# Performance work log

Measured on AMD Instinct MI355X. Metric: run time of the kernel, lower is better.

The kernel has to match this reference:

```python
import jax, jax.numpy as jnp
import numpy as np

B = 4          # clouds per batch
N_PER = 8192   # points per cloud
RATIO = 0.5
M = int(N_PER * RATIO)   # sampled centroids per cloud
R = 0.2        # radius
K = 64         # max_num_neighbors
C_IN = 64


def setup_inputs() -> dict:
    key = jax.random.key(0)
    k1, k2, k3, k4 = jax.random.split(key, 4)
    N = B * N_PER
    x = jax.random.normal(k1, (N, C_IN), dtype=jnp.float32)
    pos = jax.random.uniform(k2, (N, 3), dtype=jnp.float32)  # unit cube
    batch = jnp.repeat(jnp.arange(B, dtype=jnp.int32), N_PER)
    W1 = jax.random.normal(k3, (C_IN + 3, 64), dtype=jnp.float32) * (1.0 / np.sqrt(C_IN + 3))
    b1 = jnp.zeros((64,), dtype=jnp.float32)
    W2 = jax.random.normal(k4, (64, 128), dtype=jnp.float32) * (1.0 / np.sqrt(64))
    b2 = jnp.zeros((128,), dtype=jnp.float32)
    return {"x": x, "pos": pos, "batch": batch, "W1": W1, "b1": b1, "W2": W2, "b2": b2}


def _fps(posb):
    """Farthest point sampling, vectorized over clouds. posb: [B, n, 3] -> idx [B, M]."""
    d0 = jnp.sum((posb - posb[:, :1]) ** 2, axis=-1)  # dist^2 to seed point 0: [B, n]

    def step(dists, _):
        far = jnp.argmax(dists, axis=1)                              # [B]
        newp = jnp.take_along_axis(posb, far[:, None, None], axis=1)  # [B, 1, 3]
        d = jnp.sum((posb - newp) ** 2, axis=-1)                      # [B, n]
        return jnp.minimum(dists, d), far.astype(jnp.int32)

    _, rest = jax.lax.scan(step, d0, None, length=M - 1)  # rest: [M-1, B]
    return jnp.concatenate([jnp.zeros((B, 1), jnp.int32), rest.T], axis=1)  # [B, M]


def reference(x, pos, batch, W1, b1, W2, b2):
    posb = pos.reshape(B, N_PER, 3)
    xb = x.reshape(B, N_PER, C_IN)

    # --- fps ---
    idx = _fps(posb)                                         # [B, M]
    q = jnp.take_along_axis(posb, idx[:, :, None], axis=1)   # sampled centroids [B, M, 3]

    # --- radius query: K nearest neighbors within radius R (same cloud) ---
    d2 = jnp.sum((q[:, :, None, :] - posb[:, None, :, :]) ** 2, axis=-1)  # [B, M, n]
    neg = jnp.where(d2 <= R * R, -d2, -jnp.inf)
    vals, nbr = jax.lax.top_k(neg, K)                        # [B, M, K]
    valid = vals > -jnp.inf                                  # neighbor mask

    # --- PointNetConv: gather -> MLP -> masked max aggregation ---
    bidx = jnp.arange(B)[:, None, None]
    xj = xb[bidx, nbr]                                       # [B, M, K, C_IN]
    rel = posb[bidx, nbr] - q[:, :, None, :]                 # [B, M, K, 3]
    feat = jnp.concatenate([xj, rel], axis=-1)               # [B, M, K, C_IN+3]
    h = jax.nn.relu(feat @ W1 + b1)                          # [B, M, K, 64]
    h = jax.nn.relu(h @ W2 + b2)                             # [B, M, K, 128]
    h = jnp.where(valid[..., None], h, -jnp.inf)
    out = jnp.max(h, axis=2)                                 # [B, M, 128]; self-edge guarantees >=1 valid

    x_out = out.reshape(B * M, 128)
    pos_out = q.reshape(B * M, 3)
    batch_out = jnp.repeat(jnp.arange(B, dtype=batch.dtype), M)
    return x_out, pos_out, batch_out
```

## Files before the change

kernel.cpp:

```cpp
#include <hip/hip_runtime.h>
#include <stdint.h>

#define NPER 8192
#define NB 4
#define MPER 4096
#define MTOT (NB*MPER)
#define KNB 64
#define CIN 64
#define R2C 0.04f

#define POSOUT_OFF (MTOT*128)
#define BATCH_OFF  (MTOT*128 + MTOT*3)

#define PRE_OFF 2162688ull
#define PRE_BYTES 8388608ull

#define SSTR 34816
#define PERM_F 29200

typedef float v2f __attribute__((ext_vector_type(2)));

#define FPS_T 1024
#define PTS 8
#define NCELL 512

#define OFF_XS 0
#define OFF_YS (OFF_XS + NPER*4)
#define OFF_ZS (OFF_YS + NPER*4)
#define OFF_OS (OFF_ZS + NPER*4)
#define OFF_WIN (OFF_OS + NPER*2)
#define OFF_HIST (OFF_WIN + MPER*2)
#define OFF_SCAN (OFF_HIST + NCELL*4)
#define OFF_SLOT (OFF_SCAN + NCELL*4)
#define OFF_SID0 (OFF_SLOT + 24)
#define OFF_BSC  (OFF_SID0 + 8)
#define FPS_LDS  (OFF_BSC + NCELL*4)

template<int CTRL>
__device__ __forceinline__ unsigned dppmax(unsigned v) {
  unsigned t = (unsigned)__builtin_amdgcn_update_dpp(
      0, (int)v, CTRL, 0xf, 0xf, true);
  return v > t ? v : t;
}
__device__ __forceinline__ unsigned wave_max_u32(unsigned v) {
  v = dppmax<0x111>(v);
  v = dppmax<0x112>(v);
  v = dppmax<0x114>(v);
  v = dppmax<0x118>(v);
  v = dppmax<0x142>(v);
  v = dppmax<0x143>(v);
  return (unsigned)__builtin_amdgcn_readlane((int)v, 63);
}

__device__ __forceinline__ unsigned brick_key(unsigned c) {
  unsigned ix = c >> 6, iy = (c >> 3) & 7, iz = c & 7;
  unsigned bid = ((ix >> 2) << 3) | ((iy >> 2) << 2) | (iz >> 1);
  unsigned lid = ((ix & 3) << 3) | ((iy & 3) << 1) | (iz & 1);
  return (bid << 5) | lid;
}

__global__ __launch_bounds__(1024) void k_fps(const float* __restrict__ pos,
                                              float* __restrict__ dout)
{
#pragma clang fp contract(off)
  extern __shared__ char smem[];
  float* Xs = (float*)(smem + OFF_XS);
  float* Ys = (float*)(smem + OFF_YS);
  float* Zs = (float*)(smem + OFF_ZS);
  unsigned short* Os = (unsigned short*)(smem + OFF_OS);
  unsigned short* winb = (unsigned short*)(smem + OFF_WIN);
  unsigned* hist = (unsigned*)(smem + OFF_HIST);
  unsigned* scanb = (unsigned*)(smem + OFF_SCAN);
  unsigned long long* slot3 = (unsigned long long*)(smem + OFF_SLOT);
  unsigned* sid0p = (unsigned*)(smem + OFF_SID0);
  unsigned* bsc = (unsigned*)(smem + OFF_BSC);

  const int b = blockIdx.x;
  const int tid = threadIdx.x;
  const float* pb = pos + (size_t)b * NPER * 3;
  float* qo = dout + POSOUT_OFF + (size_t)b * MPER * 3;
  float* scrb = dout + (size_t)b * SSTR;
  float* gSX = scrb; float* gSY = scrb + 8192; float* gSZ = scrb + 16384;
  unsigned* gSO = (unsigned*)(scrb + 24576);
  unsigned* gCS = (unsigned*)(scrb + 28672);
  unsigned short* gPM = (unsigned short*)(scrb + PERM_F);

  if (tid < NCELL) hist[tid] = 0u;
  if (tid == 0) { slot3[0] = 0ull; slot3[1] = 0ull; slot3[2] = 0ull; }
  __syncthreads();

  float sxv[PTS], syv[PTS], szv[PTS];
  unsigned cellv[PTS];
#pragma unroll
  for (int k = 0; k < PTS; ++k) {
    int i = k * FPS_T + tid;
    sxv[k] = pb[i*3+0]; syv[k] = pb[i*3+1]; szv[k] = pb[i*3+2];
    unsigned ix = min(7u, (unsigned)(int)(sxv[k] * 8.0f));
    unsigned iy = min(7u, (unsigned)(int)(syv[k] * 8.0f));
    unsigned iz = min(7u, (unsigned)(int)(szv[k] * 8.0f));
    cellv[k] = (ix << 6) | (iy << 3) | iz;
    atomicAdd(&hist[cellv[k]], 1u);
  }
  __syncthreads();
  if (tid < NCELL) scanb[tid] = hist[tid];
  __syncthreads();
  for (int s = 1; s < NCELL; s <<= 1) {
    unsigned v = 0u;
    if (tid >= s && tid < NCELL) v = scanb[tid - s];
    __syncthreads();
    if (tid >= s && tid < NCELL) scanb[tid] += v;
    __syncthreads();
  }
  if (tid < NCELL) {
    hist[tid] = scanb[tid] - hist[tid];
    gCS[tid+1] = scanb[tid];
  }
  if (tid == 0) gCS[0] = 0u;
  __syncthreads();
  if (tid < NCELL) {
    unsigned c = (unsigned)tid;
    unsigned cntc = scanb[c] - hist[c];
    bsc[brick_key(c)] = cntc;
  }
  __syncthreads();
  for (int s = 1; s < NCELL; s <<= 1) {
    unsigned v = 0u;
    if (tid >= s && tid < NCELL) v = bsc[tid - s];
    __syncthreads();
    if (tid >= s && tid < NCELL) bsc[tid] += v;
    __syncthreads();
  }
  {
    unsigned bst = 0u;
    if (tid < NCELL) {
      unsigned c = (unsigned)tid;
      unsigned cntc = scanb[c] - hist[c];
      bst = bsc[brick_key(c)] - cntc;
    }
    __syncthreads();
    if (tid < NCELL) bsc[tid] = bst;
  }
  __syncthreads();
#pragma unroll
  for (int k = 0; k < PTS; ++k) {
    unsigned dst = atomicAdd(&hist[cellv[k]], 1u);
    unsigned p   = atomicAdd(&bsc[cellv[k]], 1u);
    int orig = k * FPS_T + tid;
    Xs[dst] = sxv[k]; Ys[dst] = syv[k]; Zs[dst] = szv[k];
    Os[dst] = (unsigned short)orig;
    gPM[p] = (unsigned short)dst;
    if (orig == 0) *sid0p = dst;
  }
  __syncthreads();
  for (int e = tid; e < NPER; e += FPS_T) {
    gSX[e] = Xs[e]; gSY[e] = Ys[e]; gSZ[e] = Zs[e];
  }
  for (int e = tid; e < NPER/2; e += FPS_T)
    gSO[e] = ((const unsigned*)Os)[e];
  v2f Xp[4], Yp[4], Zp[4], Dp[4];
  unsigned RK[PTS];
  float bxlo = 3.402823466e+38f, bylo = bxlo, bzlo = bxlo;
  float bxhi = -bxlo, byhi = bxhi, bzhi = bxhi;
#pragma unroll
  for (int k = 0; k < PTS; ++k) {
    int s = (int)gPM[tid * PTS + k];
    float xx = Xs[s], yy = Ys[s], zz = Zs[s];
    Xp[k>>1][k&1] = xx; Yp[k>>1][k&1] = yy; Zp[k>>1][k&1] = zz;
    Dp[k>>1][k&1] = 3.402823466e+38f;
    unsigned orig = Os[s];
    RK[k] = ((unsigned)(NPER - 1 - orig) << 13) | (unsigned)s;
    bxlo = fminf(bxlo, xx); bxhi = fmaxf(bxhi, xx);
    bylo = fminf(bylo, yy); byhi = fmaxf(byhi, yy);
    bzlo = fminf(bzlo, zz); bzhi = fmaxf(bzhi, zz);
  }

  unsigned long long tkey = 0ull, wkey = 0ull;
  float lmax = 3.402823466e+38f;
  unsigned sidx = *sid0p;
  for (int m = 1; m < MPER; ++m) {
    const float cx = Xs[sidx], cy = Ys[sidx], cz = Zs[sidx];
    if (tid == 0) winb[m-1] = (unsigned short)sidx;
    if (tid == 1) slot3[(m+1) % 3] = 0ull;
    float ax = fmaxf(fmaxf(__fsub_rn(bxlo, cx), __fsub_rn(cx, bxhi)), 0.0f);
    float ay = fmaxf(fmaxf(__fsub_rn(bylo, cy), __fsub_rn(cy, byhi)), 0.0f);
    float az = fmaxf(fmaxf(__fsub_rn(bzlo, cz), __fsub_rn(cz, bzhi)), 0.0f);
    float lb = ax*ax + ay*ay + az*az;
    bool upd = (lb * 0.99988f) < lmax;
    if (__ballot(upd) != 0ull) {
      if (upd) {
        v2f cx2 = {cx, cx}, cy2 = {cy, cy}, cz2 = {cz, cz};
        v2f dnp[4];
        float bd = -1.0f;
#pragma unroll
        for (int p = 0; p < 4; ++p) {
          v2f dx = Xp[p] - cx2;
          v2f dy = Yp[p] - cy2;
          v2f dz = Zp[p] - cz2;
          v2f s = (dx*dx + dy*dy) + dz*dz;
          v2f dn;
          dn.x = fminf(Dp[p].x, s.x);
          dn.y = fminf(Dp[p].y, s.y);
          Dp[p] = dn; dnp[p] = dn;
          bd = fmaxf(bd, fmaxf(dn.x, dn.y));
        }
        unsigned brk = 0u;
#pragma unroll
        for (int p = 0; p < 4; ++p) {
          brk = (dnp[p].x == bd) ? max(brk, RK[2*p])   : brk;
          brk = (dnp[p].y == bd) ? max(brk, RK[2*p+1]) : brk;
        }
        tkey = ((unsigned long long)__float_as_uint(bd) << 26) | brk;
        lmax = bd;
      }
      unsigned hi = (unsigned)(tkey >> 26);
      unsigned M = wave_max_u32(hi);
      unsigned rk = (unsigned)tkey & 0x3FFFFFFu;
      unsigned long long msk = __ballot(hi == M);
      unsigned lo;
      if (__popcll(msk) == 1) {
        int ln = (int)__builtin_ctzll(msk);
        lo = (unsigned)__builtin_amdgcn_readlane((int)rk, ln);
      } else {
        lo = wave_max_u32((hi == M) ? rk : 0u);
      }
      wkey = ((unsigned long long)M << 26) | lo;
    }
    if ((tid & 63) == 0) atomicMax(&slot3[m % 3], wkey);
    __syncthreads();
    sidx = (unsigned)(slot3[m % 3] & 0x1FFFull);
  }
  if (tid == 0) winb[MPER-1] = (unsigned short)sidx;
  __syncthreads();
  for (int e = tid; e < MPER; e += FPS_T) {
    unsigned s = winb[e];
    qo[e*3+0] = Xs[s]; qo[e*3+1] = Ys[s]; qo[e*3+2] = Zs[s];
  }
}

#define SCAP 512
__global__ __launch_bounds__(256) void k_radius(const float* __restrict__ pos,
    float* __restrict__ dout, unsigned short* __restrict__ nbr,
    int* __restrict__ cnt)
{
  __shared__ unsigned candH[4][SCAP];
  __shared__ unsigned candL[4][SCAP];
  const int wid = threadIdx.x >> 6, lane = threadIdx.x & 63;
  const int m = blockIdx.x * 4 + wid;
  const int b = m >> 12;
  const float* scrb = dout + (size_t)b * SSTR;
  const float* SX = scrb;
  const float* SY = scrb + 8192;
  const float* SZ = scrb + 16384;
  const unsigned short* SO = (const unsigned short*)(scrb + 24576);
  const unsigned* CS = (const unsigned*)(scrb + 28672);
  const float* q = dout + POSOUT_OFF + (size_t)m * 3;
  const float qx = q[0], qy = q[1], qz = q[2];
  const int ixc = min(7, (int)(qx * 8.0f));
  const int iyc = min(7, (int)(qy * 8.0f));
  const int izc = min(7, (int)(qz * 8.0f));
  const int izlo = max(izc-2, 0), izhi = min(izc+2, 7);
  unsigned s0v = 0u, s1v = 0u;
  {
    int ix = ixc + lane / 5 - 2;
    int iy = iyc + lane % 5 - 2;
    if (lane < 25 && ix >= 0 && ix < 8 && iy >= 0 && iy < 8) {
      int cb = (ix << 6) | (iy << 3);
      s0v = CS[cb + izlo];
      s1v = CS[cb + izhi + 1];
    }
  }
  unsigned cw = 0;
  for (int seg = 0; seg < 25; ++seg) {
    unsigned s0 = (unsigned)__builtin_amdgcn_readlane((int)s0v, seg);
    unsigned s1 = (unsigned)__builtin_amdgcn_readlane((int)s1v, seg);
    for (unsigned i0 = s0; i0 < s1; i0 += 64) {
      unsigned i = i0 + (unsigned)lane;
      float dx = __fsub_rn(qx, SX[i]);
      float dy = __fsub_rn(qy, SY[i]);
      float dz = __fsub_rn(qz, SZ[i]);
      float d2 = __fadd_rn(__fadd_rn(__fmul_rn(dx,dx), __fmul_rn(dy,dy)),
                           __fmul_rn(dz,dz));
      bool in = (i < s1) && (d2 <= R2C);
      unsigned long long mk = __ballot(in);
      unsigned pre = (unsigned)__popcll(mk & ((1ull << lane) - 1ull));
      if (in) {
        unsigned slot = cw + pre;
        if (slot < SCAP) {
          candH[wid][slot] = __float_as_uint(d2);
          candL[wid][slot] = (unsigned)SO[i];
        }
      }
      cw += (unsigned)__popcll(mk);
    }
  }
  if (cw > SCAP) cw = SCAP;
  for (int s = (int)cw + lane; s < SCAP; s += 64) {
    candH[wid][s] = 0xFFFFFFFFu; candL[wid][s] = 0xFFFFFFFFu;
  }
  __syncthreads();
  for (int k = 2; k <= SCAP; k <<= 1) {
    for (int j = k >> 1; j > 0; j >>= 1) {
#pragma unroll
      for (int s = 0; s < SCAP/128; ++s) {
        int t = lane + (s << 6);
        int e = ((t & ~(j-1)) << 1) | (t & (j-1));
        int p = e | j;
        unsigned aH = candH[wid][e], aL = candL[wid][e];
        unsigned cH = candH[wid][p], cL = candL[wid][p];
        bool agt = (aH > cH) || (aH == cH && aL > cL);
        bool asc = ((e & k) == 0);
        bool sw = asc ? agt : !agt && (aH != cH || aL != cL);
        if (sw) {
          candH[wid][e] = cH; candL[wid][e] = cL;
          candH[wid][p] = aH; candL[wid][p] = aL;
        }
      }
      __syncthreads();
    }
  }
  int kk = (int)cw; if (kk > KNB) kk = KNB;
  nbr[(size_t)m*KNB + lane] =
    (lane < kk) ? (unsigned short)(candL[wid][lane] & 0xFFFFu)
                : (unsigned short)0;
  if (lane == 0) {
    cnt[m] = kk;
    dout[BATCH_OFF + m] = (float)b;
  }
}

__global__ __launch_bounds__(256) void k_pre(const float* __restrict__ x,
    const float* __restrict__ W1, float* __restrict__ hp)
{
  __shared__ float Ws[64*64];
  __shared__ float Xs[64][65];
  const int t = threadIdx.x;
  const int row0 = blockIdx.x * 64;
  for (int e = t; e < 64*64; e += 256) Ws[e] = W1[e];
  for (int e = t; e < 64*64; e += 256) {
    int r = e >> 6, ch = e & 63;
    Xs[r][ch] = x[(size_t)(row0 + r) * 64 + ch];
  }
  __syncthreads();
  const int rg = t >> 4, cg = t & 15;
  const int r0 = rg << 2, c0 = cg << 2;
  float acc[4][4];
#pragma unroll
  for (int r = 0; r < 4; ++r)
#pragma unroll
    for (int c = 0; c < 4; ++c) acc[r][c] = 0.0f;
  for (int k = 0; k < 64; ++k) {
    const float4 w = *(const float4*)&Ws[(k << 6) + c0];
    const float xr[4] = {Xs[r0][k], Xs[r0+1][k], Xs[r0+2][k], Xs[r0+3][k]};
    const float wc[4] = {w.x, w.y, w.z, w.w};
#pragma unroll
    for (int r = 0; r < 4; ++r)
#pragma unroll
      for (int c = 0; c < 4; ++c)
        acc[r][c] = fmaf(xr[r], wc[c], acc[r][c]);
  }
#pragma unroll
  for (int r = 0; r < 4; ++r) {
    float4 o = {acc[r][0], acc[r][1], acc[r][2], acc[r][3]};
    *(float4*)&hp[(size_t)(row0 + r0 + r) * 64 + c0] = o;
  }
}

__global__ __launch_bounds__(128) void k_conv2(
    const float* __restrict__ hp, const float* __restrict__ pos,
    const float* __restrict__ W1, const float* __restrict__ b1,
    const float* __restrict__ W2, const float* __restrict__ b2,
    const unsigned short* __restrict__ nbr, const int* __restrict__ cntp,
    float* __restrict__ dout)
{
  __shared__ __align__(16) float bufA[68*68];
  __shared__ __align__(16) float bufB[16*136];
  __shared__ float w1p[3*64];
  __shared__ unsigned short nbr_s[64];
  __shared__ float qv[3];
  __shared__ int cnt_s;
  const int t = threadIdx.x;
  const int m = blockIdx.x;
  const int b = m >> 12;
  if (t < 64) nbr_s[t] = nbr[(size_t)m*KNB + t];
  else if (t == 64) cnt_s = cntp[m];
  else if (t >= 65 && t < 68) qv[t-65] = dout[POSOUT_OFF + (size_t)m*3 + (t-65)];
  for (int e = t; e < 192; e += 128) w1p[e] = W1[64*64 + e];
  __syncthreads();
  {
    const int h = t & 63, jj = t >> 6;
    const size_t hb = (size_t)b * NPER * 64;
    for (int j0 = 0; j0 < 64; j0 += 2) {
      int j = j0 + jj;
      int r = nbr_s[j];
      bufA[h*68 + j] = hp[hb + (size_t)r*64 + h];
    }
  }
  {
    const size_t pbb = (size_t)b * NPER * 3;
    for (int e = t; e < 192; e += 128) {
      int j = e & 63, d = e >> 6;
      int r = nbr_s[j];
      bufA[(64+d)*68 + j] = pos[pbb + (size_t)r*3 + d] - qv[d];
    }
  }
  __syncthreads();
  for (int e = t; e < 64*64; e += 128) {
    int h = e >> 6, j = e & 63;
    float v = bufA[h*68 + j];
    v = fmaf(bufA[64*68 + j], w1p[h],       v);
    v = fmaf(bufA[65*68 + j], w1p[64 + h],  v);
    v = fmaf(bufA[66*68 + j], w1p[128 + h], v);
    bufA[h*68 + j] = fmaxf(v + b1[h], 0.0f);
  }
  const int jg = t & 7, hg = t >> 3;
  const int j0 = jg << 3;
  const int c0 = hg << 3;
  v2f acc2p[8][4];
#pragma unroll
  for (int c = 0; c < 8; ++c)
#pragma unroll
    for (int jp = 0; jp < 4; ++jp) acc2p[c][jp] = (v2f){0.0f, 0.0f};
  for (int hc = 0; hc < 64; hc += 16) {
    __syncthreads();
    for (int e = t; e < 16*128; e += 128) {
      int hh = e >> 7, c = e & 127;
      bufB[hh*136 + c] = W2[(size_t)(hc+hh)*128 + c];
    }
    __syncthreads();
#pragma unroll
    for (int h = 0; h < 16; ++h) {
      const float4 ja = *(const float4*)&bufA[(hc+h)*68 + j0];
      const float4 jb = *(const float4*)&bufA[(hc+h)*68 + j0 + 4];
      const float4 wa = *(const float4*)&bufB[h*136 + c0];
      const float4 wb = *(const float4*)&bufB[h*136 + c0 + 4];
      const v2f hj[4] = {{ja.x, ja.y}, {ja.z, ja.w}, {jb.x, jb.y}, {jb.z, jb.w}};
      const float wv[8] = {wa.x, wa.y, wa.z, wa.w, wb.x, wb.y, wb.z, wb.w};
#pragma unroll
      for (int c = 0; c < 8; ++c) {
        const v2f w2 = {wv[c], wv[c]};
#pragma unroll
        for (int jp = 0; jp < 4; ++jp)
          acc2p[c][jp] += w2 * hj[jp];
      }
    }
  }
  const int cntv = cnt_s;
  const float4 b2a = *(const float4*)&b2[c0];
  const float4 b2b = *(const float4*)&b2[c0 + 4];
  const float bv2[8] = {b2a.x, b2a.y, b2a.z, b2a.w, b2b.x, b2b.y, b2b.z, b2b.w};
  float best[8];
#pragma unroll
  for (int c = 0; c < 8; ++c) {
    float v = -3.402823466e+38f;
#pragma unroll
    for (int jp = 0; jp < 4; ++jp) {
      float h0v = fmaxf(acc2p[c][jp].x + bv2[c], 0.0f);
      float h1v = fmaxf(acc2p[c][jp].y + bv2[c], 0.0f);
      v = (j0 + 2*jp     < cntv) ? fmaxf(v, h0v) : v;
      v = (j0 + 2*jp + 1 < cntv) ? fmaxf(v, h1v) : v;
    }
    best[c] = v;
  }
#pragma unroll
  for (int off = 1; off < 8; off <<= 1)
#pragma unroll
    for (int c = 0; c < 8; ++c)
      best[c] = fmaxf(best[c], __shfl_xor(best[c], off));
  if (jg == 0) {
    float4 o0 = {best[0], best[1], best[2], best[3]};
    float4 o1 = {best[4], best[5], best[6], best[7]};
    *(float4*)&dout[(size_t)m*128 + c0] = o0;
    *(float4*)&dout[(size_t)m*128 + c0 + 4] = o1;
  }
}

__global__ __launch_bounds__(128) void k_conv(
    const float* __restrict__ x, const float* __restrict__ pos,
    const float* __restrict__ W1, const float* __restrict__ b1,
    const float* __restrict__ W2, const float* __restrict__ b2,
    const unsigned short* __restrict__ nbr, const int* __restrict__ cntp,
    float* __restrict__ dout)
{
  __shared__ __align__(16) float bufA[68*68];
  __shared__ __align__(16) float bufB[68*68];
  __shared__ unsigned short nbr_s[64];
  __shared__ float qv[3];
  __shared__ int cnt_s;
  const int t = threadIdx.x;
  const int m = blockIdx.x;
  const int b = m >> 12;
  if (t < 64) nbr_s[t] = nbr[(size_t)m*KNB + t];
  else if (t == 64) cnt_s = cntp[m];
  else if (t >= 65 && t < 68) qv[t-65] = dout[POSOUT_OFF + (size_t)m*3 + (t-65)];
  for (int e = t; e < 67*64; e += 128) {
    int ch = e >> 6, h = e & 63;
    bufB[ch*68 + h] = W1[e];
  }
  __syncthreads();
  {
    const int ch = t & 63, jj = t >> 6;
    const size_t xb = (size_t)b * NPER * CIN;
    for (int j0 = 0; j0 < 64; j0 += 2) {
      int j = j0 + jj;
      int r = nbr_s[j];
      bufA[ch*68 + j] = x[xb + (size_t)r*CIN + ch];
    }
  }
  {
    const size_t pbb = (size_t)b * NPER * 3;
    for (int e = t; e < 192; e += 128) {
      int j = e & 63, d = e >> 6;
      int r = nbr_s[j];
      bufA[(64+d)*68 + j] = pos[pbb + (size_t)r*3 + d] - qv[d];
    }
  }
  __syncthreads();
  const int jg = t & 7, hg = t >> 3;
  const int j0 = jg << 3;
  const int h0 = hg << 2;
  v2f accp[4][4];
#pragma unroll
  for (int hh = 0; hh < 4; ++hh)
#pragma unroll
    for (int jp = 0; jp < 4; ++jp) accp[hh][jp] = (v2f){0.0f, 0.0f};
  for (int ch = 0; ch < 67; ++ch) {
    const float4 fa = *(const float4*)&bufA[ch*68 + j0];
    const float4 fb = *(const float4*)&bufA[ch*68 + j0 + 4];
    const float4 w  = *(const float4*)&bufB[ch*68 + h0];
    const v2f fj[4] = {{fa.x, fa.y}, {fa.z, fa.w}, {fb.x, fb.y}, {fb.z, fb.w}};
    const float ws4[4] = {w.x, w.y, w.z, w.w};
#pragma unroll
    for (int hh = 0; hh < 4; ++hh) {
      const v2f wv2 = {ws4[hh], ws4[hh]};
#pragma unroll
      for (int jp = 0; jp < 4; ++jp)
        accp[hh][jp] += wv2 * fj[jp];
    }
  }
  __syncthreads();
  {
    const float4 bb = *(const float4*)&b1[h0];
    const float bv[4] = {bb.x, bb.y, bb.z, bb.w};
#pragma unroll
    for (int hh = 0; hh < 4; ++hh) {
      float4 o0, o1;
      o0.x = fmaxf(accp[hh][0].x + bv[hh], 0.0f);
      o0.y = fmaxf(accp[hh][0].y + bv[hh], 0.0f);
      o0.z = fmaxf(accp[hh][1].x + bv[hh], 0.0f);
      o0.w = fmaxf(accp[hh][1].y + bv[hh], 0.0f);
      o1.x = fmaxf(accp[hh][2].x + bv[hh], 0.0f);
      o1.y = fmaxf(accp[hh][2].y + bv[hh], 0.0f);
      o1.z = fmaxf(accp[hh][3].x + bv[hh], 0.0f);
      o1.w = fmaxf(accp[hh][3].y + bv[hh], 0.0f);
      *(float4*)&bufA[(h0+hh)*68 + j0] = o0;
      *(float4*)&bufA[(h0+hh)*68 + j0 + 4] = o1;
    }
  }
  const int c0 = hg << 3;
  v2f acc2p[8][4];
#pragma unroll
  for (int c = 0; c < 8; ++c)
#pragma unroll
    for (int jp = 0; jp < 4; ++jp) acc2p[c][jp] = (v2f){0.0f, 0.0f};
  for (int hc = 0; hc < 64; hc += 16) {
    __syncthreads();
    for (int e = t; e < 16*128; e += 128) {
      int hh = e >> 7, c = e & 127;
      bufB[hh*136 + c] = W2[(size_t)(hc+hh)*128 + c];
    }
    __syncthreads();
#pragma unroll
    for (int h = 0; h < 16; ++h) {
      const float4 ja = *(const float4*)&bufA[(hc+h)*68 + j0];
      const float4 jb = *(const float4*)&bufA[(hc+h)*68 + j0 + 4];
      const float4 wa = *(const float4*)&bufB[h*136 + c0];
      const float4 wb = *(const float4*)&bufB[h*136 + c0 + 4];
      const v2f hj[4] = {{ja.x, ja.y}, {ja.z, ja.w}, {jb.x, jb.y}, {jb.z, jb.w}};
      const float wv[8] = {wa.x, wa.y, wa.z, wa.w, wb.x, wb.y, wb.z, wb.w};
#pragma unroll
      for (int c = 0; c < 8; ++c) {
        const v2f w2 = {wv[c], wv[c]};
#pragma unroll
        for (int jp = 0; jp < 4; ++jp)
          acc2p[c][jp] += w2 * hj[jp];
      }
    }
  }
  const int cntv = cnt_s;
  const float4 b2a = *(const float4*)&b2[c0];
  const float4 b2b = *(const float4*)&b2[c0 + 4];
  const float bv2[8] = {b2a.x, b2a.y, b2a.z, b2a.w, b2b.x, b2b.y, b2b.z, b2b.w};
  float best[8];
#pragma unroll
  for (int c = 0; c < 8; ++c) {
    float v = -3.402823466e+38f;
#pragma unroll
    for (int jp = 0; jp < 4; ++jp) {
      float h0v = fmaxf(acc2p[c][jp].x + bv2[c], 0.0f);
      float h1v = fmaxf(acc2p[c][jp].y + bv2[c], 0.0f);
      v = (j0 + 2*jp     < cntv) ? fmaxf(v, h0v) : v;
      v = (j0 + 2*jp + 1 < cntv) ? fmaxf(v, h1v) : v;
    }
    best[c] = v;
  }
#pragma unroll
  for (int off = 1; off < 8; off <<= 1)
#pragma unroll
    for (int c = 0; c < 8; ++c)
      best[c] = fmaxf(best[c], __shfl_xor(best[c], off));
  if (jg == 0) {
    float4 o0 = {best[0], best[1], best[2], best[3]};
    float4 o1 = {best[4], best[5], best[6], best[7]};
    *(float4*)&dout[(size_t)m*128 + c0] = o0;
    *(float4*)&dout[(size_t)m*128 + c0 + 4] = o1;
  }
}

extern "C" void kernel_launch(void* const* d_in, const int* in_sizes, int n_in,
                              void* d_out, int out_size, void* d_ws, size_t ws_size,
                              hipStream_t stream) {
  const float* x   = (const float*)d_in[0];
  const float* pos = (const float*)d_in[1];
  const float* W1  = (const float*)d_in[3];
  const float* b1  = (const float*)d_in[4];
  const float* W2  = (const float*)d_in[5];
  const float* b2  = (const float*)d_in[6];
  float* dout = (float*)d_out;
  unsigned short* nbr = (unsigned short*)d_ws;
  int* cnt = (int*)((char*)d_ws + (size_t)MTOT*KNB*2);
  float* hp = (float*)((char*)d_ws + PRE_OFF);
  const bool use_pre = (ws_size >= PRE_OFF + PRE_BYTES);

  hipLaunchKernelGGL(k_fps,    dim3(NB),     dim3(FPS_T), FPS_LDS, stream, pos, dout);
  hipLaunchKernelGGL(k_radius, dim3(MTOT/4), dim3(256),   0, stream, pos, dout, nbr, cnt);
  if (use_pre) {
    hipLaunchKernelGGL(k_pre,   dim3(NB*NPER/64), dim3(256), 0, stream, x, W1, hp);
    hipLaunchKernelGGL(k_conv2, dim3(MTOT),       dim3(128), 0, stream,
                       hp, pos, W1, b1, W2, b2, nbr, cnt, dout);
  } else {
    hipLaunchKernelGGL(k_conv,  dim3(MTOT),       dim3(128), 0, stream,
                       x, pos, W1, b1, W2, b2, nbr, cnt, dout);
  }
}
```

Before: 3.011 ms.

## Fold x·W1 precompute into FPS launch as extra blocks to overlap

The separate k_pre kernel is removed and its 64-row matmul tiles become extra blocks of the k_fps launch. Those blocks run the precompute on otherwise idle CUs while the four serial FPS blocks execute, which hides the precompute time and saves one launch. The cost is that these blocks use 1024-thread groups with only 256 threads computing and need the large FPS dynamic LDS allocation, which may limit how many are resident at once.

```diff
diff --git a/kernel.cpp b/kernel.cpp
--- a/kernel.cpp
+++ b/kernel.cpp
@@ -60,10 +60,53 @@
 }
 
 __global__ __launch_bounds__(1024) void k_fps(const float* __restrict__ pos,
-                                              float* __restrict__ dout)
+                                              float* __restrict__ dout,
+                                              const float* __restrict__ xin,
+                                              const float* __restrict__ W1,
+                                              float* __restrict__ hp)
 {
 #pragma clang fp contract(off)
   extern __shared__ char smem[];
+  const int tid = threadIdx.x;
+
+  if (blockIdx.x >= NB) {
+    float* Ws = (float*)smem;
+    float* Xs2 = (float*)(smem + 16384);
+    const int row0 = (blockIdx.x - NB) * 64;
+    for (int e = tid; e < 64*64; e += FPS_T) Ws[e] = W1[e];
+    for (int e = tid; e < 64*64; e += FPS_T) {
+      int r = e >> 6, ch = e & 63;
+      Xs2[r*65 + ch] = xin[(size_t)(row0 + r) * 64 + ch];
+    }
+    __syncthreads();
+    if (tid < 256) {
+      const int rg = tid >> 4, cg = tid & 15;
+      const int r0 = rg << 2, c0 = cg << 2;
+      float acc[4][4];
+#pragma unroll
+      for (int r = 0; r < 4; ++r)
+#pragma unroll
+        for (int c = 0; c < 4; ++c) acc[r][c] = 0.0f;
+      for (int k = 0; k < 64; ++k) {
+        const float4 w = *(const float4*)&Ws[(k << 6) + c0];
+        const float xr[4] = {Xs2[(r0+0)*65 + k], Xs2[(r0+1)*65 + k],
+                             Xs2[(r0+2)*65 + k], Xs2[(r0+3)*65 + k]};
+        const float wc[4] = {w.x, w.y, w.z, w.w};
+#pragma unroll
+        for (int r = 0; r < 4; ++r)
+#pragma unroll
+          for (int c = 0; c < 4; ++c)
+            acc[r][c] = fmaf(xr[r], wc[c], acc[r][c]);
+      }
+#pragma unroll
+      for (int r = 0; r < 4; ++r) {
+        float4 o = {acc[r][0], acc[r][1], acc[r][2], acc[r][3]};
+        *(float4*)&hp[(size_t)(row0 + r0 + r) * 64 + c0] = o;
+      }
+    }
+    return;
+  }
+
   float* Xs = (float*)(smem + OFF_XS);
   float* Ys = (float*)(smem + OFF_YS);
   float* Zs = (float*)(smem + OFF_ZS);
@@ -76,7 +119,6 @@
   unsigned* bsc = (unsigned*)(smem + OFF_BSC);
 
   const int b = blockIdx.x;
-  const int tid = threadIdx.x;
   const float* pb = pos + (size_t)b * NPER * 3;
   float* qo = dout + POSOUT_OFF + (size_t)b * MPER * 3;
   float* scrb = dout + (size_t)b * SSTR;
@@ -328,43 +370,6 @@
   }
 }
 
-__global__ __launch_bounds__(256) void k_pre(const float* __restrict__ x,
-    const float* __restrict__ W1, float* __restrict__ hp)
-{
-  __shared__ float Ws[64*64];
-  __shared__ float Xs[64][65];
-  const int t = threadIdx.x;
-  const int row0 = blockIdx.x * 64;
-  for (int e = t; e < 64*64; e += 256) Ws[e] = W1[e];
-  for (int e = t; e < 64*64; e += 256) {
-    int r = e >> 6, ch = e & 63;
-    Xs[r][ch] = x[(size_t)(row0 + r) * 64 + ch];
-  }
-  __syncthreads();
-  const int rg = t >> 4, cg = t & 15;
-  const int r0 = rg << 2, c0 = cg << 2;
-  float acc[4][4];
-#pragma unroll
-  for (int r = 0; r < 4; ++r)
-#pragma unroll
-    for (int c = 0; c < 4; ++c) acc[r][c] = 0.0f;
-  for (int k = 0; k < 64; ++k) {
-    const float4 w = *(const float4*)&Ws[(k << 6) + c0];
-    const float xr[4] = {Xs[r0][k], Xs[r0+1][k], Xs[r0+2][k], Xs[r0+3][k]};
-    const float wc[4] = {w.x, w.y, w.z, w.w};
-#pragma unroll
-    for (int r = 0; r < 4; ++r)
-#pragma unroll
-      for (int c = 0; c < 4; ++c)
-        acc[r][c] = fmaf(xr[r], wc[c], acc[r][c]);
-  }
-#pragma unroll
-  for (int r = 0; r < 4; ++r) {
-    float4 o = {acc[r][0], acc[r][1], acc[r][2], acc[r][3]};
-    *(float4*)&hp[(size_t)(row0 + r0 + r) * 64 + c0] = o;
-  }
-}
-
 __global__ __launch_bounds__(128) void k_conv2(
     const float* __restrict__ hp, const float* __restrict__ pos,
     const float* __restrict__ W1, const float* __restrict__ b1,
@@ -631,10 +636,11 @@
   float* hp = (float*)((char*)d_ws + PRE_OFF);
   const bool use_pre = (ws_size >= PRE_OFF + PRE_BYTES);
 
-  hipLaunchKernelGGL(k_fps,    dim3(NB),     dim3(FPS_T), FPS_LDS, stream, pos, dout);
+  const int grid = use_pre ? (NB + NB*NPER/64) : NB;
+  hipLaunchKernelGGL(k_fps,    dim3(grid),   dim3(FPS_T), FPS_LDS, stream,
+                     pos, dout, x, W1, hp);
   hipLaunchKernelGGL(k_radius, dim3(MTOT/4), dim3(256),   0, stream, pos, dout, nbr, cnt);
   if (use_pre) {
-    hipLaunchKernelGGL(k_pre,   dim3(NB*NPER/64), dim3(256), 0, stream, x, W1, hp);
     hipLaunchKernelGGL(k_conv2, dim3(MTOT),       dim3(128), 0, stream,
                        hp, pos, W1, b1, W2, b2, nbr, cnt, dout);
   } else {
```

New measurement: 2.929 ms, median of 2. -2.7%, faster.
